# Kernel optimization log

Measured on AMD Instinct MI355X. Metric: run time of the kernel, lower is better.

The kernel has to match this reference:

```python
import jax, jax.numpy as jnp
import numpy as np

EMBED = 192
D_INNER = 2 * EMBED          # expand=2
D_STATE = 4                  # low_rank
D_CONV = 4
DT_RANK = (EMBED + 15) // 16 # ceil(192/16) = 12
N_MIX = 2
RANK = 4                     # LowRankProjection rank
B_, H_, W_ = 8, 64, 64


def setup_inputs() -> dict:
    key = jax.random.key(0)
    ks = jax.random.split(key, 16)
    s = lambda *sh: 1.0 / np.sqrt(sh[-1])
    inp = {
        "x": jax.random.normal(ks[0], (B_, EMBED, H_, W_), jnp.float32),
        # stacked per-mixer Mamba params (leading dim N_MIX)
        "in_proj_w": jax.random.normal(ks[1], (N_MIX, 2 * D_INNER, EMBED), jnp.float32) * s(EMBED),
        "conv_w": jax.random.normal(ks[2], (N_MIX, D_INNER, D_CONV), jnp.float32) * s(D_CONV),
        "conv_b": jnp.zeros((N_MIX, D_INNER), jnp.float32),
        "x_proj_w": jax.random.normal(ks[3], (N_MIX, DT_RANK + 2 * D_STATE, D_INNER), jnp.float32) * s(D_INNER),
        "dt_proj_w": jax.random.normal(ks[4], (N_MIX, D_INNER, DT_RANK), jnp.float32) * s(DT_RANK),
        "dt_proj_b": jax.random.uniform(ks[5], (N_MIX, D_INNER), jnp.float32, -4.0, -2.0),
        "A_log": jnp.tile(jnp.log(jnp.arange(1, D_STATE + 1, dtype=jnp.float32))[None, None, :], (N_MIX, D_INNER, 1)),
        "D": jnp.ones((N_MIX, D_INNER), jnp.float32),
        "out_proj_w": jax.random.normal(ks[6], (N_MIX, EMBED, D_INNER), jnp.float32) * s(D_INNER),
        # LowRankProjection
        "U_w": jax.random.normal(ks[7], (RANK, EMBED), jnp.float32) * s(EMBED),
        "V_w": jax.random.normal(ks[8], (EMBED, RANK), jnp.float32) * s(RANK),
        # LayerNorm
        "ln_g": jnp.ones((EMBED,), jnp.float32),
        "ln_b": jnp.zeros((EMBED,), jnp.float32),
    }
    return inp


def _silu(x):
    return x * jax.nn.sigmoid(x)


def _mamba(x, in_proj_w, conv_w, conv_b, x_proj_w, dt_proj_w, dt_proj_b, A_log, D, out_proj_w):
    # x: (B, L, d_model)
    B, L, _ = x.shape
    xz = jnp.einsum("bld,ed->ble", x, in_proj_w)          # (B, L, 2*d_inner)
    xin, z = jnp.split(xz, 2, axis=-1)
    # causal depthwise conv over L
    xt = jnp.transpose(xin, (0, 2, 1))                      # (B, d_inner, L)
    xc = jax.lax.conv_general_dilated(
        xt, conv_w[:, None, :], window_strides=(1,), padding=[(D_CONV - 1, 0)],
        feature_group_count=D_INNER, dimension_numbers=("NCH", "OIH", "NCH"))
    xa = _silu(jnp.transpose(xc + conv_b[None, :, None], (0, 2, 1)))  # (B, L, d_inner)
    x_dbl = jnp.einsum("bld,ed->ble", xa, x_proj_w)         # (B, L, dt_rank+2*d_state)
    dt_lr = x_dbl[..., :DT_RANK]
    Bm = x_dbl[..., DT_RANK:DT_RANK + D_STATE]              # (B, L, d_state)
    Cm = x_dbl[..., DT_RANK + D_STATE:]                     # (B, L, d_state)
    dt = jax.nn.softplus(jnp.einsum("blr,dr->bld", dt_lr, dt_proj_w) + dt_proj_b)  # (B, L, d_inner)
    A = -jnp.exp(A_log)                                     # (d_inner, d_state)
    dA = jnp.exp(dt[..., None] * A)                         # (B, L, d_inner, d_state)
    dBu = dt[..., None] * Bm[:, :, None, :] * xa[..., None]  # (B, L, d_inner, d_state)

    def step(h, inputs):
        dA_i, dBu_i, C_i = inputs                           # (B,d_inner,d_state),(B,d_inner,d_state),(B,d_state)
        h = dA_i * h + dBu_i
        y = jnp.einsum("bds,bs->bd", h, C_i)
        return h, y

    h0 = jnp.zeros((B, D_INNER, D_STATE), x.dtype)
    _, ys = jax.lax.scan(step, h0, (jnp.moveaxis(dA, 1, 0), jnp.moveaxis(dBu, 1, 0), jnp.moveaxis(Cm, 1, 0)))
    y = jnp.moveaxis(ys, 0, 1) + xa * D                     # (B, L, d_inner)
    y = y * _silu(z)
    return jnp.einsum("ble,de->bld", y, out_proj_w)         # (B, L, d_model)


def reference(x, in_proj_w, conv_w, conv_b, x_proj_w, dt_proj_w, dt_proj_b,
              A_log, D, out_proj_w, U_w, V_w, ln_g, ln_b):
    residual = x
    B, C, H, W = x.shape
    h = jnp.transpose(x, (0, 2, 3, 1)).reshape(B, H * W, C)
    for i in range(N_MIX):
        h = _mamba(h, in_proj_w[i], conv_w[i], conv_b[i], x_proj_w[i], dt_proj_w[i],
                   dt_proj_b[i], A_log[i], D[i], out_proj_w[i])
    # low-rank projection
    h = jnp.einsum("blr,dr->bld", jnp.einsum("blc,rc->blr", h, U_w), V_w)
    h = jnp.transpose(h.reshape(B, H, W, C), (0, 3, 1, 2)) + residual
    # LayerNorm over channels
    hc = jnp.transpose(h, (0, 2, 3, 1))
    mu = hc.mean(-1, keepdims=True)
    var = ((hc - mu) ** 2).mean(-1, keepdims=True)
    hc = (hc - mu) * jax.lax.rsqrt(var + 1e-5) * ln_g + ln_b
    return jnp.transpose(hc, (0, 3, 1, 2))
```

## Files before the change

kernel.cpp:

```cpp
#include <hip/hip_runtime.h>
#include <hip/hip_bf16.h>
#include <cstdint>

#define EMBED   192
#define DINNER  384
#define DSTATE  4
#define DCONV   4
#define DTRANK  12
#define NMIX    2
#define RANK    4
#define BB      8
#define LL      4096
#define NBL     (BB*LL)
#define NCHUNK  128
#define CLEN    32
#define RSTR    36

typedef __attribute__((ext_vector_type(8))) short short8;
typedef __attribute__((ext_vector_type(4))) float float4v;

static __device__ __forceinline__ ushort f2b(float f) {
    __hip_bfloat16 h = __float2bfloat16(f);
    return *(ushort*)&h;
}
static __device__ __forceinline__ float b2f(ushort u) {
    __hip_bfloat16 h;
    *(ushort*)&h = u;
    return __bfloat162float(h);
}
static __device__ __forceinline__ float bs2f(short s) {
    ushort u = (ushort)s;
    return b2f(u);
}

#define PREP_N0 294912
#define PREP_N1 147456
#define PREP_N2 24576
#define PREP_N3 24576
#define PREP_N4 3072
__global__ __launch_bounds__(256) void k_prep(const float* __restrict__ in_proj_w,
                                              const float* __restrict__ out_proj_w,
                                              const float* __restrict__ x_proj_w,
                                              const float* __restrict__ dt_proj_w,
                                              const float* __restrict__ conv_w,
                                              ushort* __restrict__ wi,
                                              ushort* __restrict__ wo,
                                              ushort* __restrict__ xpwb,
                                              ushort* __restrict__ dtwpad,
                                              float* __restrict__ cwt) {
    int i = blockIdx.x * 256 + threadIdx.x;
    if (i < PREP_N0) {
        wi[i] = f2b(in_proj_w[i]);
        return;
    }
    i -= PREP_N0;
    if (i < PREP_N1) {
        wo[i] = f2b(out_proj_w[i]);
        return;
    }
    i -= PREP_N1;
    if (i < PREP_N2) {
        int mix = i / (32 * 384);
        int rem = i % (32 * 384);
        int e = rem / 384, k = rem % 384;
        xpwb[i] = (e < 20) ? f2b(x_proj_w[(size_t)mix * 20 * 384 + e * 384 + k]) : (ushort)0;
        return;
    }
    i -= PREP_N2;
    if (i < PREP_N3) {
        int mix = i / (384 * 32);
        int rem = i % (384 * 32);
        int n = rem / 32, r = rem % 32;
        dtwpad[i] = (r < DTRANK) ? f2b(dt_proj_w[(size_t)mix * 384 * DTRANK + n * DTRANK + r])
                                 : (ushort)0;
        return;
    }
    i -= PREP_N3;
    if (i < PREP_N4) {
        int mix = i / (DCONV * DINNER);
        int rem = i % (DCONV * DINNER);
        int k = rem / DINNER, d = rem % DINNER;
        cwt[i] = conv_w[(size_t)mix * DINNER * DCONV + d * DCONV + k];
    }
}

__global__ __launch_bounds__(256) void k_transpose(const float* __restrict__ x,
                                                   ushort* __restrict__ h0b) {
    __shared__ float tile[32][33];
    int b  = blockIdx.z;
    int c0 = blockIdx.y * 32;
    int l0 = blockIdx.x * 32;
    int tx = threadIdx.x;
    int ty = threadIdx.y;
    #pragma unroll
    for (int i = 0; i < 4; i++) {
        int c = c0 + ty + i * 8;
        tile[ty + i * 8][tx] = x[((size_t)b * EMBED + c) * LL + l0 + tx];
    }
    __syncthreads();
    #pragma unroll
    for (int i = 0; i < 4; i++) {
        int l = l0 + ty + i * 8;
        h0b[((size_t)b * LL + l) * EMBED + c0 + tx] = f2b(tile[tx][ty + i * 8]);
    }
}

template<int TN, int WRN, bool SILUZ>
__global__ __launch_bounds__(256) void k_gemm_bf16(const ushort* __restrict__ A, int lda,
                                                   const ushort* __restrict__ Bw, int ldb,
                                                   ushort* __restrict__ Cb, int ldcb,
                                                   int K) {
    constexpr int WRM = 4 / WRN;
    constexpr int WM  = 128 / WRM;
    constexpr int MT  = WM / 16;
    constexpr int NBU = TN / 64;
    __shared__ ushort As[2][128][40];
    __shared__ ushort Bs[2][TN][40];
    int tid  = threadIdx.x;
    int lane = tid & 63;
    int wave = tid >> 6;
    int mcol = lane & 15;
    int quad = lane >> 4;
    int wmo = (wave / WRN) * WM;
    int wno = (wave % WRN) * 64;
    int m0 = blockIdx.x * 128;
    int n0 = blockIdx.y * TN;

    float4v acc[MT][4];
    #pragma unroll
    for (int i = 0; i < MT; i++)
        #pragma unroll
        for (int j = 0; j < 4; j++)
            acc[i][j] = (float4v){0.f, 0.f, 0.f, 0.f};

    short8 pa[2], pb[NBU];
    #pragma unroll
    for (int i = 0; i < 2; i++) {
        int idx = tid + i * 256, r = idx >> 2, sg = idx & 3;
        pa[i] = *(const short8*)(A + (size_t)(m0 + r) * lda + sg * 8);
    }
    #pragma unroll
    for (int i = 0; i < NBU; i++) {
        int idx = tid + i * 256, r = idx >> 2, sg = idx & 3;
        pb[i] = *(const short8*)(Bw + (size_t)(n0 + r) * ldb + sg * 8);
    }
    #pragma unroll
    for (int i = 0; i < 2; i++) {
        int idx = tid + i * 256;
        *(short8*)&As[0][idx >> 2][(idx & 3) * 8] = pa[i];
    }
    #pragma unroll
    for (int i = 0; i < NBU; i++) {
        int idx = tid + i * 256;
        *(short8*)&Bs[0][idx >> 2][(idx & 3) * 8] = pb[i];
    }
    __syncthreads();

    int cur = 0;
    for (int k0 = 0; k0 < K; k0 += 32) {
        bool more = (k0 + 32) < K;
        if (more) {
            #pragma unroll
            for (int i = 0; i < 2; i++) {
                int idx = tid + i * 256, r = idx >> 2, sg = idx & 3;
                pa[i] = *(const short8*)(A + (size_t)(m0 + r) * lda + k0 + 32 + sg * 8);
            }
            #pragma unroll
            for (int i = 0; i < NBU; i++) {
                int idx = tid + i * 256, r = idx >> 2, sg = idx & 3;
                pb[i] = *(const short8*)(Bw + (size_t)(n0 + r) * ldb + k0 + 32 + sg * 8);
            }
        }
        short8 av[MT], bv[4];
        #pragma unroll
        for (int i = 0; i < MT; i++)
            av[i] = *(const short8*)&As[cur][wmo + i * 16 + mcol][quad * 8];
        #pragma unroll
        for (int j = 0; j < 4; j++)
            bv[j] = *(const short8*)&Bs[cur][wno + j * 16 + mcol][quad * 8];
        #pragma unroll
        for (int i = 0; i < MT; i++)
            #pragma unroll
            for (int j = 0; j < 4; j++)
                acc[i][j] = __builtin_amdgcn_mfma_f32_16x16x32_bf16(
                    av[i], bv[j], acc[i][j], 0, 0, 0);
        if (more) {
            #pragma unroll
            for (int i = 0; i < 2; i++) {
                int idx = tid + i * 256;
                *(short8*)&As[cur ^ 1][idx >> 2][(idx & 3) * 8] = pa[i];
            }
            #pragma unroll
            for (int i = 0; i < NBU; i++) {
                int idx = tid + i * 256;
                *(short8*)&Bs[cur ^ 1][idx >> 2][(idx & 3) * 8] = pb[i];
            }
        }
        __syncthreads();
        cur ^= 1;
    }

    #pragma unroll
    for (int i = 0; i < MT; i++) {
        int rbase = m0 + wmo + i * 16 + quad * 4;
        #pragma unroll
        for (int j = 0; j < 4; j++) {
            int col = n0 + wno + j * 16 + mcol;
            #pragma unroll
            for (int r = 0; r < 4; r++) {
                float v = acc[i][j][r];
                if (SILUZ && col >= DINNER) v = v / (1.f + __expf(-v));
                Cb[(size_t)(rbase + r) * ldcb + col] = f2b(v);
            }
        }
    }
}

__global__ __launch_bounds__(256) void k_conv_silu(const ushort* __restrict__ xz,
                                                   const float* __restrict__ cwt,
                                                   const float* __restrict__ cb,
                                                   ushort* __restrict__ xa) {
    int t   = blockIdx.x * 256 + threadIdx.x;
    int g   = t % 48;
    int blc = t / 48;
    int d0  = g * 8;
    int lc  = blc % (LL / 8);
    int b   = blc / (LL / 8);
    int l0  = lc * 8;

    float wk[4][8], bias[8];
    #pragma unroll
    for (int k = 0; k < 4; k++) {
        float4v wa = *(const float4v*)(cwt + k * DINNER + d0);
        float4v wb = *(const float4v*)(cwt + k * DINNER + d0 + 4);
        #pragma unroll
        for (int j = 0; j < 4; j++) { wk[k][j] = wa[j]; wk[k][j + 4] = wb[j]; }
    }
    {
        float4v ba = *(const float4v*)(cb + d0);
        float4v bb = *(const float4v*)(cb + d0 + 4);
        #pragma unroll
        for (int j = 0; j < 4; j++) { bias[j] = ba[j]; bias[j + 4] = bb[j]; }
    }

    float r0[8] = {}, r1[8] = {}, r2[8] = {};
    const ushort* px = xz + ((size_t)(b * LL + l0)) * 768 + d0;
    if (l0 > 0) {
        short8 v;
        v = *(const short8*)(px - 3 * 768);
        #pragma unroll
        for (int j = 0; j < 8; j++) r0[j] = bs2f(v[j]);
        v = *(const short8*)(px - 2 * 768);
        #pragma unroll
        for (int j = 0; j < 8; j++) r1[j] = bs2f(v[j]);
        v = *(const short8*)(px - 1 * 768);
        #pragma unroll
        for (int j = 0; j < 8; j++) r2[j] = bs2f(v[j]);
    }
    ushort* po = xa + ((size_t)(b * LL + l0)) * DINNER + d0;
    #pragma unroll
    for (int i = 0; i < 8; i++) {
        short8 v = *(const short8*)(px + (size_t)i * 768);
        float cur[8];
        #pragma unroll
        for (int j = 0; j < 8; j++) cur[j] = bs2f(v[j]);
        short8 ov;
        #pragma unroll
        for (int j = 0; j < 8; j++) {
            float a = bias[j] + wk[0][j] * r0[j] + wk[1][j] * r1[j]
                    + wk[2][j] * r2[j] + wk[3][j] * cur[j];
            float sv = a / (1.f + __expf(-a));
            ov[j] = (short)f2b(sv);
        }
        *(short8*)(po + (size_t)i * DINNER) = ov;
        #pragma unroll
        for (int j = 0; j < 8; j++) { r0[j] = r1[j]; r1[j] = r2[j]; r2[j] = cur[j]; }
    }
}

__global__ __launch_bounds__(256) void k_xproj_mfma(const ushort* __restrict__ xa,
                                                    const ushort* __restrict__ xpwb,
                                                    float* __restrict__ xdb32) {
    __shared__ ushort As[128][40];
    __shared__ ushort Bs[32][40];
    int tid  = threadIdx.x;
    int lane = tid & 63;
    int wave = tid >> 6;
    int m0 = blockIdx.x * 128;
    float4v acc[2][2];
    #pragma unroll
    for (int i = 0; i < 2; i++)
        #pragma unroll
        for (int j = 0; j < 2; j++)
            acc[i][j] = (float4v){0.f, 0.f, 0.f, 0.f};
    for (int k0 = 0; k0 < 384; k0 += 32) {
        #pragma unroll
        for (int i = 0; i < 2; i++) {
            int idx = tid + i * 256;
            int r = idx >> 2, sg = idx & 3;
            *(short8*)&As[r][sg * 8] =
                *(const short8*)(xa + (size_t)(m0 + r) * 384 + k0 + sg * 8);
        }
        if (tid < 128) {
            int r = tid >> 2, sg = tid & 3;
            *(short8*)&Bs[r][sg * 8] =
                *(const short8*)(xpwb + (size_t)r * 384 + k0 + sg * 8);
        }
        __syncthreads();
        short8 av[2], bv[2];
        #pragma unroll
        for (int i = 0; i < 2; i++)
            av[i] = *(const short8*)&As[wave * 32 + i * 16 + (lane & 15)][(lane >> 4) * 8];
        #pragma unroll
        for (int j = 0; j < 2; j++)
            bv[j] = *(const short8*)&Bs[j * 16 + (lane & 15)][(lane >> 4) * 8];
        #pragma unroll
        for (int i = 0; i < 2; i++)
            #pragma unroll
            for (int j = 0; j < 2; j++)
                acc[i][j] = __builtin_amdgcn_mfma_f32_16x16x32_bf16(
                    av[i], bv[j], acc[i][j], 0, 0, 0);
        __syncthreads();
    }
    #pragma unroll
    for (int i = 0; i < 2; i++) {
        int rbase = m0 + wave * 32 + i * 16 + (lane >> 4) * 4;
        #pragma unroll
        for (int j = 0; j < 2; j++) {
            int col = j * 16 + (lane & 15);
            #pragma unroll
            for (int r = 0; r < 4; r++)
                xdb32[(size_t)(rbase + r) * 32 + col] = acc[i][j][r];
        }
    }
}

static __device__ __forceinline__ void dt_mfma_tile(const float* __restrict__ rows,
                                                    const ushort* __restrict__ dtwpad,
                                                    const float* __restrict__ dtb,
                                                    ushort* __restrict__ dtS,
                                                    int wave, int lane) {
    int mcol = lane & 15;
    int quad = lane >> 4;
    #pragma unroll
    for (int nt = 0; nt < 4; nt++) {
        int n = wave * 64 + nt * 16 + mcol;
        short8 bv = *(const short8*)(dtwpad + (size_t)n * 32 + quad * 8);
        float bias = dtb[n];
        #pragma unroll
        for (int mt = 0; mt < 2; mt++) {
            float4v a0 = *(const float4v*)&rows[(mt * 16 + mcol) * RSTR + quad * 8];
            float4v a1 = *(const float4v*)&rows[(mt * 16 + mcol) * RSTR + quad * 8 + 4];
            short8 av;
            #pragma unroll
            for (int j = 0; j < 4; j++) {
                av[j]     = (short)f2b(a0[j]);
                av[j + 4] = (short)f2b(a1[j]);
            }
            float4v acc = (float4v){0.f, 0.f, 0.f, 0.f};
            acc = __builtin_amdgcn_mfma_f32_16x16x32_bf16(av, bv, acc, 0, 0, 0);
            #pragma unroll
            for (int r = 0; r < 4; r++) {
                float s = acc[r] + bias;
                float sp = fmaxf(s, 0.f) + __logf(1.f + __expf(-fabsf(s)));
                dtS[(mt * 16 + quad * 4 + r) * DINNER + n] = f2b(sp);
            }
        }
    }
}

static __device__ __forceinline__ bool as_is_harmonic(const float* As) {
    return fabsf(As[1] - 2.f * As[0]) <= 1e-5f * fabsf(As[1]) + 1e-12f
        && fabsf(As[2] - 3.f * As[0]) <= 1e-5f * fabsf(As[2]) + 1e-12f
        && fabsf(As[3] - 4.f * As[0]) <= 1e-5f * fabsf(As[3]) + 1e-12f;
}

__global__ __launch_bounds__(384) void k_scan_local(const ushort* __restrict__ xa,
                                                    const float* __restrict__ xdb32,
                                                    const ushort* __restrict__ dtwpad,
                                                    const float* __restrict__ dtb,
                                                    const float* __restrict__ A_log,
                                                    const float* __restrict__ Dp,
                                                    float* __restrict__ carryT,
                                                    float* __restrict__ carryH,
                                                    uint* __restrict__ dyb) {
    int d     = threadIdx.x;
    int lane  = d & 63;
    int wave  = d >> 6;
    int chunk = blockIdx.x;
    int b     = blockIdx.y;
    __shared__ float rows[CLEN * RSTR];
    __shared__ ushort dtS[CLEN * DINNER];
    size_t rbase = ((size_t)b * LL + (size_t)chunk * CLEN) * 32;
    for (int i = d; i < CLEN * 32; i += 384) {
        int l = i >> 5, e = i & 31;
        rows[l * RSTR + e] = xdb32[rbase + i];
    }
    float As[DSTATE];
    #pragma unroll
    for (int s = 0; s < DSTATE; s++) As[s] = -__expf(A_log[d * DSTATE + s]);
    bool fastA = as_is_harmonic(As);
    float Dd = Dp[d];
    __syncthreads();
    dt_mfma_tile(rows, dtwpad, dtb, dtS, wave, lane);
    __syncthreads();
    float h[DSTATE] = {0.f, 0.f, 0.f, 0.f};
    float T = 0.f;
    size_t mbase = (size_t)b * LL + (size_t)chunk * CLEN;
    #pragma unroll 8
    for (int l = 0; l < CLEN; l++) {
        ushort dtu = dtS[l * DINNER + d];
        float dtvv = b2f(dtu);
        float xav  = b2f(xa[(mbase + l) * DINNER + d]);
        float du   = dtvv * xav;
        T += dtvv;
        const float* row = &rows[l * RSTR];
        float da[DSTATE];
        if (fastA) {
            float p = __expf(dtvv * As[0]);
            da[0] = p; da[1] = p * p; da[2] = da[1] * p; da[3] = da[2] * p;
        } else {
            #pragma unroll
            for (int s = 0; s < DSTATE; s++) da[s] = __expf(dtvv * As[s]);
        }
        float yv = xav * Dd;
        #pragma unroll
        for (int s = 0; s < DSTATE; s++) {
            h[s] = da[s] * h[s] + du * row[DTRANK + s];
            yv  += h[s] * row[DTRANK + DSTATE + s];
        }
        dyb[(mbase + l) * DINNER + d] = ((uint)dtu << 16) | (uint)f2b(yv);
    }
    size_t cb = ((size_t)chunk * BB + b);
    carryT[cb * 384 + d] = T;
    float4v hv = {h[0], h[1], h[2], h[3]};
    *(float4v*)(carryH + cb * 1536 + d * 4) = hv;
}

__global__ __launch_bounds__(256) void k_scan_combine(const float* __restrict__ carryT,
                                                      const float* __restrict__ carryH,
                                                      const float* __restrict__ A_log,
                                                      float* __restrict__ carryI) {
    int c   = blockIdx.x * 256 + threadIdx.x;
    int b   = c / 1536;
    int rem = c - b * 1536;
    int d   = rem >> 2;
    float As = -__expf(A_log[rem]);
    float hrun = 0.f;
    #pragma unroll 4
    for (int k = 0; k < NCHUNK; k++) {
        size_t o = (size_t)k * BB + b;
        float T  = carryT[o * 384 + d];
        float Hk = carryH[o * 1536 + rem];
        carryI[o * 1536 + rem] = hrun;
        hrun = __expf(As * T) * hrun + Hk;
    }
}

__global__ __launch_bounds__(384) void k_scan_corr(const uint* __restrict__ dyb,
                                                   const ushort* __restrict__ xz,
                                                   const float* __restrict__ xdb32,
                                                   const float* __restrict__ A_log,
                                                   const float* __restrict__ carryI,
                                                   ushort* __restrict__ y) {
    int d     = threadIdx.x;
    int chunk = blockIdx.x;
    int b     = blockIdx.y;
    __shared__ float Crow[CLEN][DSTATE];
    size_t rbase = ((size_t)b * LL + (size_t)chunk * CLEN) * 32;
    if (d < CLEN * DSTATE) {
        int l = d >> 2, s = d & 3;
        Crow[l][s] = xdb32[rbase + l * 32 + DTRANK + DSTATE + s];
    }
    float As[DSTATE];
    #pragma unroll
    for (int s = 0; s < DSTATE; s++) As[s] = -__expf(A_log[d * DSTATE + s]);
    bool fastA = as_is_harmonic(As);
    float4v hv = *(const float4v*)(carryI + ((size_t)chunk * BB + b) * 1536 + d * 4);
    float hc[DSTATE];
    #pragma unroll
    for (int s = 0; s < DSTATE; s++) hc[s] = hv[s];
    __syncthreads();
    size_t mbase = (size_t)b * LL + (size_t)chunk * CLEN;
    #pragma unroll 8
    for (int l = 0; l < CLEN; l++) {
        size_t m = mbase + l;
        uint dv = dyb[m * DINNER + d];
        float dtvv = b2f((ushort)(dv >> 16));
        float ylv  = b2f((ushort)(dv & 0xffffu));
        float da[DSTATE];
        if (fastA) {
            float p = __expf(dtvv * As[0]);
            da[0] = p; da[1] = p * p; da[2] = da[1] * p; da[3] = da[2] * p;
        } else {
            #pragma unroll
            for (int s = 0; s < DSTATE; s++) da[s] = __expf(dtvv * As[s]);
        }
        float corr = 0.f;
        #pragma unroll
        for (int s = 0; s < DSTATE; s++) {
            hc[s] *= da[s];
            corr  += hc[s] * Crow[l][s];
        }
        float yv = ylv + corr;
        float zs = b2f(xz[m * 768 + DINNER + d]);
        yv *= zs;
        y[m * DINNER + d] = f2b(yv);
    }
}

__global__ __launch_bounds__(256) void k_tail(const ushort* __restrict__ h1b,
                                              const ushort* __restrict__ h0b,
                                              const float* __restrict__ U,
                                              const float* __restrict__ V,
                                              const float* __restrict__ g,
                                              const float* __restrict__ be,
                                              float* __restrict__ out) {
    __shared__ float tile[EMBED * 65];
    int tid  = threadIdx.x;
    int lane = tid & 63;
    int wave = tid >> 6;
    int b  = blockIdx.y;
    int l0 = blockIdx.x * 64;
    for (int t = 0; t < 16; t++) {
        int lloc = wave * 16 + t;
        size_t m = (size_t)b * LL + l0 + lloc;
        float hv[3];
        #pragma unroll
        for (int i = 0; i < 3; i++) hv[i] = b2f(h1b[m * EMBED + lane + 64 * i]);
        float r[RANK];
        #pragma unroll
        for (int j = 0; j < RANK; j++) {
            float p = 0.f;
            #pragma unroll
            for (int i = 0; i < 3; i++) p += hv[i] * U[j * EMBED + lane + 64 * i];
            #pragma unroll
            for (int off = 1; off < 64; off <<= 1) p += __shfl_xor(p, off);
            r[j] = p;
        }
        float u[3], s1 = 0.f, s2 = 0.f;
        #pragma unroll
        for (int i = 0; i < 3; i++) {
            int c = lane + 64 * i;
            float v = r[0] * V[c * 4 + 0] + r[1] * V[c * 4 + 1]
                    + r[2] * V[c * 4 + 2] + r[3] * V[c * 4 + 3];
            u[i] = v + b2f(h0b[m * EMBED + c]);
            s1 += u[i];
            s2 += u[i] * u[i];
        }
        #pragma unroll
        for (int off = 1; off < 64; off <<= 1) {
            s1 += __shfl_xor(s1, off);
            s2 += __shfl_xor(s2, off);
        }
        float mean = s1 * (1.f / EMBED);
        float var  = s2 * (1.f / EMBED) - mean * mean;
        float inv  = rsqrtf(var + 1e-5f);
        #pragma unroll
        for (int i = 0; i < 3; i++) {
            int c = lane + 64 * i;
            tile[c * 65 + lloc] = (u[i] - mean) * inv * g[c] + be[c];
        }
    }
    __syncthreads();
    for (int i = tid; i < EMBED * 64; i += 256) {
        int c = i >> 6, l = i & 63;
        out[((size_t)(b * EMBED + c)) * LL + l0 + l] = tile[c * 65 + l];
    }
}

extern "C" void kernel_launch(void* const* d_in, const int* in_sizes, int n_in,
                              void* d_out, int out_size, void* d_ws, size_t ws_size,
                              hipStream_t stream) {
    const float* x          = (const float*)d_in[0];
    const float* in_proj_w  = (const float*)d_in[1];
    const float* conv_w     = (const float*)d_in[2];
    const float* conv_b     = (const float*)d_in[3];
    const float* x_proj_w   = (const float*)d_in[4];
    const float* dt_proj_w  = (const float*)d_in[5];
    const float* dt_proj_b  = (const float*)d_in[6];
    const float* A_log      = (const float*)d_in[7];
    const float* Dp         = (const float*)d_in[8];
    const float* out_proj_w = (const float*)d_in[9];
    const float* U_w        = (const float*)d_in[10];
    const float* V_w        = (const float*)d_in[11];
    const float* ln_g       = (const float*)d_in[12];
    const float* ln_b       = (const float*)d_in[13];
    float* out = (float*)d_out;

    float* ws    = (float*)d_ws;
    float* xdb32 = ws;
    float* carryT = xdb32 + (size_t)NBL * 32;
    float* carryH = carryT + (size_t)NCHUNK * BB * DINNER;
    float* carryI = carryH + (size_t)NCHUNK * BB * DINNER * DSTATE;
    ushort* xz16   = (ushort*)(carryI + (size_t)NCHUNK * BB * DINNER * DSTATE);
    ushort* xa16   = xz16   + (size_t)NBL * 768;
    ushort* yb     = xa16   + (size_t)NBL * DINNER;
    ushort* h0b    = yb     + (size_t)NBL * DINNER;
    ushort* h1b    = h0b    + (size_t)NBL * EMBED;
    uint*   dyb    = (uint*)(h1b + (size_t)NBL * EMBED);
    ushort* wi     = (ushort*)(dyb + (size_t)NBL * DINNER);
    ushort* wo     = wi     + (size_t)NMIX * 768 * EMBED;
    ushort* xpwb   = wo     + (size_t)NMIX * EMBED * DINNER;
    ushort* dtwpad = xpwb   + (size_t)NMIX * 32 * 384;
    float*  cwt    = (float*)(dtwpad + (size_t)NMIX * 384 * 32);

    k_prep<<<(PREP_N0 + PREP_N1 + PREP_N2 + PREP_N3 + PREP_N4) / 256, 256, 0, stream>>>(
        in_proj_w, out_proj_w, x_proj_w, dt_proj_w, conv_w, wi, wo, xpwb, dtwpad, cwt);

    k_transpose<<<dim3(LL / 32, EMBED / 32, BB), dim3(32, 8), 0, stream>>>(x, h0b);

    const ushort* hinb = h0b;
    for (int mix = 0; mix < NMIX; mix++) {
        const float* Alg  = A_log + (size_t)mix * DINNER * DSTATE;
        const ushort* dtwm = dtwpad + (size_t)mix * 384 * 32;
        const float* dtbm = dt_proj_b + mix * DINNER;

        k_gemm_bf16<128, 2, true><<<dim3(NBL / 128, 768 / 128), 256, 0, stream>>>(
            hinb, EMBED, wi + (size_t)mix * 768 * EMBED, EMBED, xz16, 768, EMBED);
        k_conv_silu<<<(NBL / 8 * 48) / 256, 256, 0, stream>>>(
            xz16, cwt + (size_t)mix * DCONV * DINNER, conv_b + mix * DINNER, xa16);
        k_xproj_mfma<<<NBL / 128, 256, 0, stream>>>(
            xa16, xpwb + (size_t)mix * 32 * 384, xdb32);
        k_scan_local<<<dim3(NCHUNK, BB), 384, 0, stream>>>(
            xa16, xdb32, dtwm, dtbm, Alg, Dp + mix * DINNER, carryT, carryH, dyb);
        k_scan_combine<<<(BB * DINNER * DSTATE) / 256, 256, 0, stream>>>(
            carryT, carryH, Alg, carryI);
        k_scan_corr<<<dim3(NCHUNK, BB), 384, 0, stream>>>(
            dyb, xz16, xdb32, Alg, carryI, yb);
        k_gemm_bf16<64, 1, false><<<dim3(NBL / 128, EMBED / 64), 256, 0, stream>>>(
            yb, DINNER, wo + (size_t)mix * EMBED * DINNER, DINNER, h1b, EMBED, DINNER);
        hinb = h1b;
    }

    k_tail<<<dim3(LL / 64, BB), 256, 0, stream>>>(h1b, h0b, U_w, V_w, ln_g, ln_b, out);
}
```

Before: 369.6 us.

## Fuse x_proj GEMM into local scan kernel via shared-memory xa tile

Removes the separate x_proj MFMA kernel. k_scan_local now stages its 32-row chunk of xa into shared memory, computes the 32-wide x_proj output with MFMA on four waves, and reuses the staged xa in the scan loop. Only the C columns are written to a compact buffer for k_scan_corr. This saves a kernel launch and the xdb32 round trip through global memory, plus the scan's repeated global reads of xa. The cost is about 25KB more shared memory per block, which may lower occupancy, and x_proj runs serially inside the scan block.

```diff
diff --git a/kernel.cpp b/kernel.cpp
--- a/kernel.cpp
+++ b/kernel.cpp
@@ -15,6 +15,7 @@
 #define NCHUNK  128
 #define CLEN    32
 #define RSTR    36
+#define XSTR    392
 
 typedef __attribute__((ext_vector_type(8))) short short8;
 typedef __attribute__((ext_vector_type(4))) float float4v;
@@ -278,63 +279,6 @@
     }
 }
 
-__global__ __launch_bounds__(256) void k_xproj_mfma(const ushort* __restrict__ xa,
-                                                    const ushort* __restrict__ xpwb,
-                                                    float* __restrict__ xdb32) {
-    __shared__ ushort As[128][40];
-    __shared__ ushort Bs[32][40];
-    int tid  = threadIdx.x;
-    int lane = tid & 63;
-    int wave = tid >> 6;
-    int m0 = blockIdx.x * 128;
-    float4v acc[2][2];
-    #pragma unroll
-    for (int i = 0; i < 2; i++)
-        #pragma unroll
-        for (int j = 0; j < 2; j++)
-            acc[i][j] = (float4v){0.f, 0.f, 0.f, 0.f};
-    for (int k0 = 0; k0 < 384; k0 += 32) {
-        #pragma unroll
-        for (int i = 0; i < 2; i++) {
-            int idx = tid + i * 256;
-            int r = idx >> 2, sg = idx & 3;
-            *(short8*)&As[r][sg * 8] =
-                *(const short8*)(xa + (size_t)(m0 + r) * 384 + k0 + sg * 8);
-        }
-        if (tid < 128) {
-            int r = tid >> 2, sg = tid & 3;
-            *(short8*)&Bs[r][sg * 8] =
-                *(const short8*)(xpwb + (size_t)r * 384 + k0 + sg * 8);
-        }
-        __syncthreads();
-        short8 av[2], bv[2];
-        #pragma unroll
-        for (int i = 0; i < 2; i++)
-            av[i] = *(const short8*)&As[wave * 32 + i * 16 + (lane & 15)][(lane >> 4) * 8];
-        #pragma unroll
-        for (int j = 0; j < 2; j++)
-            bv[j] = *(const short8*)&Bs[j * 16 + (lane & 15)][(lane >> 4) * 8];
-        #pragma unroll
-        for (int i = 0; i < 2; i++)
-            #pragma unroll
-            for (int j = 0; j < 2; j++)
-                acc[i][j] = __builtin_amdgcn_mfma_f32_16x16x32_bf16(
-                    av[i], bv[j], acc[i][j], 0, 0, 0);
-        __syncthreads();
-    }
-    #pragma unroll
-    for (int i = 0; i < 2; i++) {
-        int rbase = m0 + wave * 32 + i * 16 + (lane >> 4) * 4;
-        #pragma unroll
-        for (int j = 0; j < 2; j++) {
-            int col = j * 16 + (lane & 15);
-            #pragma unroll
-            for (int r = 0; r < 4; r++)
-                xdb32[(size_t)(rbase + r) * 32 + col] = acc[i][j][r];
-        }
-    }
-}
-
 static __device__ __forceinline__ void dt_mfma_tile(const float* __restrict__ rows,
                                                     const ushort* __restrict__ dtwpad,
                                                     const float* __restrict__ dtb,
@@ -376,25 +320,29 @@
 }
 
 __global__ __launch_bounds__(384) void k_scan_local(const ushort* __restrict__ xa,
-                                                    const float* __restrict__ xdb32,
+                                                    const ushort* __restrict__ xpwb,
                                                     const ushort* __restrict__ dtwpad,
                                                     const float* __restrict__ dtb,
                                                     const float* __restrict__ A_log,
                                                     const float* __restrict__ Dp,
                                                     float* __restrict__ carryT,
                                                     float* __restrict__ carryH,
+                                                    float* __restrict__ ccol,
                                                     uint* __restrict__ dyb) {
     int d     = threadIdx.x;
     int lane  = d & 63;
     int wave  = d >> 6;
     int chunk = blockIdx.x;
     int b     = blockIdx.y;
+    __shared__ ushort xaS[CLEN][XSTR];
     __shared__ float rows[CLEN * RSTR];
     __shared__ ushort dtS[CLEN * DINNER];
-    size_t rbase = ((size_t)b * LL + (size_t)chunk * CLEN) * 32;
-    for (int i = d; i < CLEN * 32; i += 384) {
-        int l = i >> 5, e = i & 31;
-        rows[l * RSTR + e] = xdb32[rbase + i];
+    size_t mbase = (size_t)b * LL + (size_t)chunk * CLEN;
+
+    for (int u = d; u < CLEN * 48; u += 384) {
+        int l = u / 48, c8 = u - l * 48;
+        *(short8*)&xaS[l][c8 * 8] =
+            *(const short8*)(xa + (mbase + l) * DINNER + c8 * 8);
     }
     float As[DSTATE];
     #pragma unroll
@@ -402,16 +350,37 @@
     bool fastA = as_is_harmonic(As);
     float Dd = Dp[d];
     __syncthreads();
+
+    if (wave < 4) {
+        int mi = wave >> 1, ni = wave & 1;
+        int mcol = lane & 15, quad = lane >> 4;
+        float4v acc = (float4v){0.f, 0.f, 0.f, 0.f};
+        #pragma unroll
+        for (int k0 = 0; k0 < 384; k0 += 32) {
+            short8 av = *(const short8*)&xaS[mi * 16 + mcol][k0 + quad * 8];
+            short8 bv = *(const short8*)(xpwb + (size_t)(ni * 16 + mcol) * 384
+                                         + k0 + quad * 8);
+            acc = __builtin_amdgcn_mfma_f32_16x16x32_bf16(av, bv, acc, 0, 0, 0);
+        }
+        #pragma unroll
+        for (int r = 0; r < 4; r++)
+            rows[(mi * 16 + quad * 4 + r) * RSTR + ni * 16 + mcol] = acc[r];
+    }
+    __syncthreads();
+    if (d < CLEN * DSTATE) {
+        int l = d >> 2, s = d & 3;
+        ccol[(mbase + l) * 4 + s] = rows[l * RSTR + DTRANK + DSTATE + s];
+    }
     dt_mfma_tile(rows, dtwpad, dtb, dtS, wave, lane);
     __syncthreads();
+
     float h[DSTATE] = {0.f, 0.f, 0.f, 0.f};
     float T = 0.f;
-    size_t mbase = (size_t)b * LL + (size_t)chunk * CLEN;
     #pragma unroll 8
     for (int l = 0; l < CLEN; l++) {
         ushort dtu = dtS[l * DINNER + d];
         float dtvv = b2f(dtu);
-        float xav  = b2f(xa[(mbase + l) * DINNER + d]);
+        float xav  = b2f(xaS[l][d]);
         float du   = dtvv * xav;
         T += dtvv;
         const float* row = &rows[l * RSTR];
@@ -459,7 +428,7 @@
 
 __global__ __launch_bounds__(384) void k_scan_corr(const uint* __restrict__ dyb,
                                                    const ushort* __restrict__ xz,
-                                                   const float* __restrict__ xdb32,
+                                                   const float* __restrict__ ccol,
                                                    const float* __restrict__ A_log,
                                                    const float* __restrict__ carryI,
                                                    ushort* __restrict__ y) {
@@ -467,10 +436,9 @@
     int chunk = blockIdx.x;
     int b     = blockIdx.y;
     __shared__ float Crow[CLEN][DSTATE];
-    size_t rbase = ((size_t)b * LL + (size_t)chunk * CLEN) * 32;
+    size_t mbase = (size_t)b * LL + (size_t)chunk * CLEN;
     if (d < CLEN * DSTATE) {
-        int l = d >> 2, s = d & 3;
-        Crow[l][s] = xdb32[rbase + l * 32 + DTRANK + DSTATE + s];
+        Crow[d >> 2][d & 3] = ccol[mbase * 4 + d];
     }
     float As[DSTATE];
     #pragma unroll
@@ -481,7 +449,6 @@
     #pragma unroll
     for (int s = 0; s < DSTATE; s++) hc[s] = hv[s];
     __syncthreads();
-    size_t mbase = (size_t)b * LL + (size_t)chunk * CLEN;
     #pragma unroll 8
     for (int l = 0; l < CLEN; l++) {
         size_t m = mbase + l;
@@ -589,8 +556,8 @@
     float* out = (float*)d_out;
 
     float* ws    = (float*)d_ws;
-    float* xdb32 = ws;
-    float* carryT = xdb32 + (size_t)NBL * 32;
+    float* ccol  = ws;
+    float* carryT = ws + (size_t)NBL * 32;
     float* carryH = carryT + (size_t)NCHUNK * BB * DINNER;
     float* carryI = carryH + (size_t)NCHUNK * BB * DINNER * DSTATE;
     ushort* xz16   = (ushort*)(carryI + (size_t)NCHUNK * BB * DINNER * DSTATE);
@@ -620,14 +587,13 @@
             hinb, EMBED, wi + (size_t)mix * 768 * EMBED, EMBED, xz16, 768, EMBED);
         k_conv_silu<<<(NBL / 8 * 48) / 256, 256, 0, stream>>>(
             xz16, cwt + (size_t)mix * DCONV * DINNER, conv_b + mix * DINNER, xa16);
-        k_xproj_mfma<<<NBL / 128, 256, 0, stream>>>(
-            xa16, xpwb + (size_t)mix * 32 * 384, xdb32);
         k_scan_local<<<dim3(NCHUNK, BB), 384, 0, stream>>>(
-            xa16, xdb32, dtwm, dtbm, Alg, Dp + mix * DINNER, carryT, carryH, dyb);
+            xa16, xpwb + (size_t)mix * 32 * 384, dtwm, dtbm, Alg,
+            Dp + mix * DINNER, carryT, carryH, ccol, dyb);
         k_scan_combine<<<(BB * DINNER * DSTATE) / 256, 256, 0, stream>>>(
             carryT, carryH, Alg, carryI);
         k_scan_corr<<<dim3(NCHUNK, BB), 384, 0, stream>>>(
-            dyb, xz16, xdb32, Alg, carryI, yb);
+            dyb, xz16, ccol, Alg, carryI, yb);
         k_gemm_bf16<64, 1, false><<<dim3(NBL / 128, EMBED / 64), 256, 0, stream>>>(
             yb, DINNER, wo + (size_t)mix * EMBED * DINNER, DINNER, h1b, EMBED, DINNER);
         hinb = h1b;
```

Result: no change. 373.0 us (+0.9%).
